# Kernel tuning notes

Measured on AMD Instinct MI355X. Metric: run time of the kernel, lower is better.

Reference implementation:

```python
import jax, jax.numpy as jnp
import numpy as np

TEMPERATURE = 0.5
EPS = 1e-12  # torch F.normalize eps


def _l2_normalize(x, eps=EPS):
    n = jnp.linalg.norm(x, axis=1, keepdims=True)
    return x / jnp.maximum(n, eps)


def setup_inputs() -> dict:
    key = jax.random.key(0)
    k1, k2 = jax.random.split(key)
    B, D = 4096, 512
    return {
        "polyline_embs": jax.random.normal(k1, (B, D), dtype=jnp.float32),
        "c_embs": jax.random.normal(k2, (B, D), dtype=jnp.float32),
    }


def reference(polyline_embs, c_embs):
    b = polyline_embs.shape[0]
    # double-normalization in the original (F.normalize then cosine_similarity)
    # is idempotent on unit vectors, so sim = Z @ Z^T with Z unit-normalized.
    z = _l2_normalize(jnp.concatenate([polyline_embs, c_embs], axis=0))  # [2B, D]
    sim = z @ z.T  # [2B, 2B] cosine similarity
    # positives: diag offsets +B and -B
    idx = jnp.arange(b)
    sim_ij = sim[idx, idx + b]
    sim_ji = sim[idx + b, idx]
    positives = jnp.concatenate([sim_ij, sim_ji], axis=0)  # [2B]
    nominator = jnp.exp(positives / TEMPERATURE)
    mask = 1.0 - jnp.eye(2 * b, dtype=sim.dtype)
    denominator = jnp.sum(mask * jnp.exp(sim / TEMPERATURE), axis=1)  # [2B]
    all_losses = -jnp.log(nominator / denominator)
    return jnp.sum(all_losses) / (2 * b)
```

## Files before the change

kernel.cpp:

```cpp
#include <hip/hip_runtime.h>
#include <hip/hip_bf16.h>

#define B_ROWS 4096
#define D_DIM  512
#define N_ROWS 8192
#define BM 128
#define BN 128
#define BKB 128
#define NBLK (N_ROWS / BM)
#define NPAIR (NBLK * (NBLK + 1) / 2)

typedef float f32x4 __attribute__((ext_vector_type(4)));
typedef int   v4i   __attribute__((ext_vector_type(4)));
typedef int   v8i   __attribute__((ext_vector_type(8)));

__device__ __forceinline__ float dpp_xor1_add(float v) {
    return v + __int_as_float(__builtin_amdgcn_mov_dpp(
        __float_as_int(v), 0xB1, 0xf, 0xf, true));
}
__device__ __forceinline__ float dpp_xor2_add(float v) {
    return v + __int_as_float(__builtin_amdgcn_mov_dpp(
        __float_as_int(v), 0x4E, 0xf, 0xf, true));
}
__device__ __forceinline__ float dpp_ror4_add(float v) {
    return v + __int_as_float(__builtin_amdgcn_mov_dpp(
        __float_as_int(v), 0x124, 0xf, 0xf, true));
}
__device__ __forceinline__ float dpp_ror8_add(float v) {
    return v + __int_as_float(__builtin_amdgcn_mov_dpp(
        __float_as_int(v), 0x128, 0xf, 0xf, true));
}

__global__ __launch_bounds__(256) void prep_kernel(
    const float* __restrict__ poly, const float* __restrict__ cemb,
    unsigned char* __restrict__ Z, float* __restrict__ row_sum,
    float* __restrict__ pos, unsigned int* __restrict__ counter)
{
    const int wave = threadIdx.x >> 6;
    const int lane = threadIdx.x & 63;
    const int r = blockIdx.x * 4 + wave;

    const float4* prow = (const float4*)(poly + (size_t)r * D_DIM) + lane * 2;
    const float4* crow = (const float4*)(cemb + (size_t)r * D_DIM) + lane * 2;
    const float4 p0 = prow[0], p1 = prow[1];
    const float4 c0 = crow[0], c1 = crow[1];

    float ssp = p0.x*p0.x + p0.y*p0.y + p0.z*p0.z + p0.w*p0.w
              + p1.x*p1.x + p1.y*p1.y + p1.z*p1.z + p1.w*p1.w;
    float ssc = c0.x*c0.x + c0.y*c0.y + c0.z*c0.z + c0.w*c0.w
              + c1.x*c1.x + c1.y*c1.y + c1.z*c1.z + c1.w*c1.w;
    float dt  = p0.x*c0.x + p0.y*c0.y + p0.z*c0.z + p0.w*c0.w
              + p1.x*c1.x + p1.y*c1.y + p1.z*c1.z + p1.w*c1.w;

    #pragma unroll
    for (int m = 1; m < 64; m <<= 1) {
        ssp += __shfl_xor(ssp, m);
        ssc += __shfl_xor(ssc, m);
        dt  += __shfl_xor(dt,  m);
    }

    const float sp = 1.0f / fmaxf(sqrtf(ssp), 1e-12f);
    const float sc = 1.0f / fmaxf(sqrtf(ssc), 1e-12f);

    int2 zp, zc;
    zp.x = __builtin_amdgcn_cvt_pk_fp8_f32(p0.x*sp, p0.y*sp, 0, false)
         | (__builtin_amdgcn_cvt_pk_fp8_f32(p0.z*sp, p0.w*sp, 0, false) << 16);
    zp.y = __builtin_amdgcn_cvt_pk_fp8_f32(p1.x*sp, p1.y*sp, 0, false)
         | (__builtin_amdgcn_cvt_pk_fp8_f32(p1.z*sp, p1.w*sp, 0, false) << 16);
    zc.x = __builtin_amdgcn_cvt_pk_fp8_f32(c0.x*sc, c0.y*sc, 0, false)
         | (__builtin_amdgcn_cvt_pk_fp8_f32(c0.z*sc, c0.w*sc, 0, false) << 16);
    zc.y = __builtin_amdgcn_cvt_pk_fp8_f32(c1.x*sc, c1.y*sc, 0, false)
         | (__builtin_amdgcn_cvt_pk_fp8_f32(c1.z*sc, c1.w*sc, 0, false) << 16);

    *(int2*)(Z + (size_t)r * D_DIM + lane * 8)            = zp;
    *(int2*)(Z + (size_t)(r + B_ROWS) * D_DIM + lane * 8) = zc;

    if (lane == 0) {
        pos[r] = dt * sp * sc;
        row_sum[2 * r]     = 0.0f;
        row_sum[2 * r + 1] = 0.0f;
        if (r == 0) *counter = 0u;
    }
}

__global__ __launch_bounds__(256) void sim_kernel(
    const unsigned char* __restrict__ Z, float* __restrict__ row_sum,
    const float* __restrict__ pos, float* __restrict__ out,
    unsigned int* __restrict__ counter)
{
    __shared__ __align__(16) unsigned char As[BM * BKB];
    __shared__ __align__(16) unsigned char Bs[BN * BKB];
    __shared__ __align__(8)  float rP[BM][2];
    __shared__ __align__(8)  float cP[BN][2];
    __shared__ unsigned int lastFlag;

    const int t0 = blockIdx.x;
    int bi = (int)((129.0f - sqrtf(16641.0f - 8.0f * (float)t0)) * 0.5f);
    #define CFN(b) ((b) * (129 - (b)) / 2)
    while (CFN(bi + 1) <= t0) ++bi;
    while (CFN(bi) > t0) --bi;
    const int bj = bi + (t0 - CFN(bi));
    #undef CFN
    const bool diag = (bi == bj);

    const int ibase = bi * BM;
    const int jbase = bj * BN;
    const int tid   = threadIdx.x;

    const int srow = tid >> 3;
    const int gchk = (tid & 7) ^ (srow & 7);

    const int wave = tid >> 6;
    const int lane = tid & 63;
    const int wi = (wave >> 1) * 64;
    const int wj = (wave & 1) * 64;
    const int quad = lane >> 4;
    const int c    = lane & 15;

    f32x4 acc[4][4] = {};

    const int sg0 = (((quad << 1)    ) ^ (c & 7)) * 16;
    const int sg1 = (((quad << 1) | 1) ^ (c & 7)) * 16;

    #pragma unroll 1
    for (int k0 = 0; k0 < D_DIM; k0 += BKB) {
        #pragma unroll
        for (int it = 0; it < 4; ++it) {
            const int row = it * 32 + srow;
            const unsigned char* ga = Z + (size_t)(ibase + row) * D_DIM + k0 + gchk * 16;
            __builtin_amdgcn_global_load_lds(
                (const __attribute__((address_space(1))) void*)ga,
                (__attribute__((address_space(3))) void*)(As + it * 4096 + tid * 16),
                16, 0, 0);
        }
        if (!diag) {
            #pragma unroll
            for (int it = 0; it < 4; ++it) {
                const int row = it * 32 + srow;
                const unsigned char* gb = Z + (size_t)(jbase + row) * D_DIM + k0 + gchk * 16;
                __builtin_amdgcn_global_load_lds(
                    (const __attribute__((address_space(1))) void*)gb,
                    (__attribute__((address_space(3))) void*)(Bs + it * 4096 + tid * 16),
                    16, 0, 0);
            }
        }
        __syncthreads();

        const unsigned char* bb = diag ? As : Bs;

        v8i bfr[4];
        #pragma unroll
        for (int tj = 0; tj < 4; ++tj) {
            const unsigned char* base = bb + (wj + tj * 16 + c) * BKB;
            const v4i lo = *(const v4i*)(base + sg0);
            const v4i hi = *(const v4i*)(base + sg1);
            bfr[tj] = __builtin_shufflevector(lo, hi, 0, 1, 2, 3, 4, 5, 6, 7);
        }
        #pragma unroll
        for (int ti = 0; ti < 4; ++ti) {
            const unsigned char* base = As + (wi + ti * 16 + c) * BKB;
            const v4i lo = *(const v4i*)(base + sg0);
            const v4i hi = *(const v4i*)(base + sg1);
            const v8i afr = __builtin_shufflevector(lo, hi, 0, 1, 2, 3, 4, 5, 6, 7);
            #pragma unroll
            for (int tj = 0; tj < 4; ++tj)
                acc[ti][tj] = __builtin_amdgcn_mfma_scale_f32_16x16x128_f8f6f4(
                    afr, bfr[tj], acc[ti][tj],
                    0, 0,
                    0, 0x7f7f7f7f,
                    0, 0x7f7f7f7f);
        }
        __syncthreads();
    }

    const float K2 = 2.885390081777927f;
    const int g = wave & 1;
    const int h = wave >> 1;
    float col[4] = {0.0f, 0.0f, 0.0f, 0.0f};

    #pragma unroll
    for (int ti = 0; ti < 4; ++ti) {
        const int li = wi + ti * 16 + quad * 4;
        #pragma unroll
        for (int r = 0; r < 4; ++r) {
            float v = 0.0f;
            if (diag) {
                const int gi = ibase + li + r;
                #pragma unroll
                for (int tj = 0; tj < 4; ++tj) {
                    const int gj = jbase + wj + tj * 16 + c;
                    const float e = (gj > gi) ? exp2f(K2 * acc[ti][tj][r]) : 0.0f;
                    v += e;
                    col[tj] += e;
                }
            } else {
                #pragma unroll
                for (int tj = 0; tj < 4; ++tj) {
                    const float e = exp2f(K2 * acc[ti][tj][r]);
                    v += e;
                    col[tj] += e;
                }
            }
            v = dpp_xor1_add(v);
            v = dpp_xor2_add(v);
            v = dpp_ror4_add(v);
            v = dpp_ror8_add(v);
            if (c == 0)
                rP[li + r][g] = v;
        }
    }
    #pragma unroll
    for (int tj = 0; tj < 4; ++tj) {
        float w = col[tj];
        w += __shfl_xor(w, 16);
        w += __shfl_xor(w, 32);
        if (quad == 0)
            cP[wj + tj * 16 + c][h] = w;
    }
    __syncthreads();

    if (tid < BM) {
        const float2 rp = *(const float2*)rP[tid];
        atomicAdd(&row_sum[ibase + tid], rp.x + rp.y);
    } else {
        const float2 cp = *(const float2*)cP[tid - BM];
        atomicAdd(&row_sum[jbase + tid - BM], cp.x + cp.y);
    }

    __syncthreads();
    if (tid == 0) {
        unsigned int old = __hip_atomic_fetch_add(
            counter, 1u, __ATOMIC_RELAXED, __HIP_MEMORY_SCOPE_AGENT);
        lastFlag = (old == NPAIR - 1) ? 1u : 0u;
    }
    __syncthreads();
    if (lastFlag) {
        float accL = 0.0f, accP = 0.0f;
        for (int i = tid; i < N_ROWS; i += 256) {
            const float rs = __hip_atomic_load(
                &row_sum[i], __ATOMIC_RELAXED, __HIP_MEMORY_SCOPE_AGENT);
            accL += __logf(rs);
        }
        for (int r = tid; r < B_ROWS; r += 256)
            accP += pos[r];
        #pragma unroll
        for (int m = 1; m < 64; m <<= 1) {
            accL += __shfl_xor(accL, m);
            accP += __shfl_xor(accP, m);
        }
        if (lane == 0) { rP[wave][0] = accL; cP[wave][0] = accP; }
        __syncthreads();
        if (tid == 0) {
            float L = 0.0f, P = 0.0f;
            #pragma unroll
            for (int w = 0; w < 4; ++w) { L += rP[w][0]; P += cP[w][0]; }
            out[0] = (L - 4.0f * P) / (float)N_ROWS;
        }
    }
}

extern "C" void kernel_launch(void* const* d_in, const int* in_sizes, int n_in,
                              void* d_out, int out_size, void* d_ws, size_t ws_size,
                              hipStream_t stream) {
    const float* poly = (const float*)d_in[0];
    const float* cemb = (const float*)d_in[1];

    unsigned char* Z       = (unsigned char*)d_ws;
    float*         row_sum = (float*)((char*)d_ws + (size_t)N_ROWS * D_DIM);
    float*         pos     = row_sum + N_ROWS;
    unsigned int*  counter = (unsigned int*)(pos + B_ROWS);
    float*         out     = (float*)d_out;

    prep_kernel<<<B_ROWS / 4, 256, 0, stream>>>(poly, cemb, Z, row_sum, pos, counter);
    sim_kernel<<<NPAIR, 256, 0, stream>>>(Z, row_sum, pos, out, counter);
}
```

Baseline: 124.2 us.

## Double-buffer LDS tiles to overlap global loads with MFMA compute

Result: no change. 123.7 us (-0.4%).

```diff
diff --git a/kernel.cpp b/kernel.cpp
--- a/kernel.cpp
+++ b/kernel.cpp
@@ -88,8 +88,8 @@
     const float* __restrict__ pos, float* __restrict__ out,
     unsigned int* __restrict__ counter)
 {
-    __shared__ __align__(16) unsigned char As[BM * BKB];
-    __shared__ __align__(16) unsigned char Bs[BN * BKB];
+    __shared__ __align__(16) unsigned char As[2][BM * BKB];
+    __shared__ __align__(16) unsigned char Bs[2][BN * BKB];
     __shared__ __align__(8)  float rP[BM][2];
     __shared__ __align__(8)  float cP[BN][2];
     __shared__ unsigned int lastFlag;
@@ -122,15 +122,14 @@
     const int sg0 = (((quad << 1)    ) ^ (c & 7)) * 16;
     const int sg1 = (((quad << 1) | 1) ^ (c & 7)) * 16;
 
-    #pragma unroll 1
-    for (int k0 = 0; k0 < D_DIM; k0 += BKB) {
+    auto stage = [&](int buf, int k0) {
         #pragma unroll
         for (int it = 0; it < 4; ++it) {
             const int row = it * 32 + srow;
             const unsigned char* ga = Z + (size_t)(ibase + row) * D_DIM + k0 + gchk * 16;
             __builtin_amdgcn_global_load_lds(
                 (const __attribute__((address_space(1))) void*)ga,
-                (__attribute__((address_space(3))) void*)(As + it * 4096 + tid * 16),
+                (__attribute__((address_space(3))) void*)(&As[buf][it * 4096 + tid * 16]),
                 16, 0, 0);
         }
         if (!diag) {
@@ -140,13 +139,29 @@
                 const unsigned char* gb = Z + (size_t)(jbase + row) * D_DIM + k0 + gchk * 16;
                 __builtin_amdgcn_global_load_lds(
                     (const __attribute__((address_space(1))) void*)gb,
-                    (__attribute__((address_space(3))) void*)(Bs + it * 4096 + tid * 16),
+                    (__attribute__((address_space(3))) void*)(&Bs[buf][it * 4096 + tid * 16]),
                     16, 0, 0);
             }
         }
-        __syncthreads();
-
-        const unsigned char* bb = diag ? As : Bs;
+    };
+
+    stage(0, 0);
+
+    #pragma unroll 1
+    for (int t = 0; t < 4; ++t) {
+        if (t < 3) stage((t + 1) & 1, (t + 1) * BKB);
+
+        if (t < 3) {
+            if (diag) asm volatile("s_waitcnt vmcnt(4)" ::: "memory");
+            else      asm volatile("s_waitcnt vmcnt(8)" ::: "memory");
+        } else {
+            asm volatile("s_waitcnt vmcnt(0)" ::: "memory");
+        }
+        __builtin_amdgcn_s_barrier();
+        __builtin_amdgcn_sched_barrier(0);
+
+        const unsigned char* ab = As[t & 1];
+        const unsigned char* bb = diag ? ab : Bs[t & 1];
 
         v8i bfr[4];
         #pragma unroll
@@ -158,7 +173,7 @@
         }
         #pragma unroll
         for (int ti = 0; ti < 4; ++ti) {
-            const unsigned char* base = As + (wi + ti * 16 + c) * BKB;
+            const unsigned char* base = ab + (wi + ti * 16 + c) * BKB;
             const v4i lo = *(const v4i*)(base + sg0);
             const v4i hi = *(const v4i*)(base + sg1);
             const v8i afr = __builtin_shufflevector(lo, hi, 0, 1, 2, 3, 4, 5, 6, 7);
@@ -170,7 +185,9 @@
                     0, 0x7f7f7f7f,
                     0, 0x7f7f7f7f);
         }
-        __syncthreads();
+
+        asm volatile("s_waitcnt lgkmcnt(0)" ::: "memory");
+        __builtin_amdgcn_s_barrier();
     }
 
     const float K2 = 2.885390081777927f;
```
